# Optimization experiments

Measured on AMD Instinct MI355X. Metric: run time of the kernel, lower is better.

## Reference

```python
import jax, jax.numpy as jnp
import numpy as np

B, L, D, H = 4, 4096, 1024, 16
Dh = D // H
DECAY_INIT, DECAY_RANGE = 5.0, 1.0
LN_EPS = 1e-5


def setup_inputs() -> dict:
    key = jax.random.key(0)
    ks = jax.random.split(key, 5)
    s = 1.0 / np.sqrt(D)
    x = jax.random.normal(ks[0], (B, L, D), dtype=jnp.float32)
    Wq = jax.random.normal(ks[1], (D, D), dtype=jnp.float32) * s
    Wv = jax.random.normal(ks[2], (D, D), dtype=jnp.float32) * s
    Wo = jax.random.normal(ks[3], (D, D), dtype=jnp.float32) * s
    Wg = jax.random.normal(ks[4], (D, D), dtype=jnp.float32) * s
    # per-head decay logits, matching __init__: 5.0 + 1.0 * h / H
    beta = DECAY_INIT + DECAY_RANGE * (jnp.arange(H, dtype=jnp.float32) / H)
    ln_gamma = jnp.ones((D,), dtype=jnp.float32)
    ln_beta = jnp.zeros((D,), dtype=jnp.float32)
    return {"x": x, "Wq": Wq, "Wv": Wv, "Wo": Wo, "Wg": Wg,
            "beta": beta, "ln_gamma": ln_gamma, "ln_beta": ln_beta}


def _retention_scan(v, lam):
    # v: (B,L,H,Dh), lam: (H,); s_t = lam * s_{t-1} + v_t  (s_{-1} = 0)
    a = jnp.broadcast_to(lam[None, None, :, None], v.shape)

    def combine(c1, c2):
        a1, b1 = c1
        a2, b2 = c2
        return a1 * a2, a2 * b1 + b2

    _, s = jax.lax.associative_scan(combine, (a, v), axis=1)
    return s


def _layernorm(x, gamma, beta):
    mu = jnp.mean(x, axis=-1, keepdims=True)
    var = jnp.mean(jnp.square(x - mu), axis=-1, keepdims=True)
    return (x - mu) * jax.lax.rsqrt(var + LN_EPS) * gamma + beta


def reference(x, Wq, Wv, Wo, Wg, beta, ln_gamma, ln_beta):
    b, l, d = x.shape
    # decay lambda per head: (1 - 2^-beta) clamped to (tiny, 1 - 1e-9)
    tiny = jnp.finfo(jnp.float32).tiny
    lam = jnp.clip(1.0 - jnp.exp2(-beta), tiny, 1.0 - 1e-9)
    q = (x @ Wq.T).reshape(b, l, H, Dh)
    v = (x @ Wv.T).reshape(b, l, H, Dh)
    state = _retention_scan(v, lam)             # (B,L,H,Dh)
    ret = (q * state).reshape(b, l, d)          # per-timestep retention readout
    y = _layernorm(ret, ln_gamma, ln_beta)
    g = jax.nn.silu(x @ Wg.T)                   # swish gate
    out = (y * g) @ Wo.T
    return out
```

## Files before the change

### kernel.cpp

```cpp
#include <hip/hip_runtime.h>
#include <hip/hip_bf16.h>
#include <cfloat>

#define BB 4
#define LL 4096
#define DD 1024
#define HH 16
#define DHH 64
#define MM (BB * LL)
#define LN_EPS 1e-5f
#define LDQVG 3072
#define SCC 16
#define NCHUNK (LL / SCC)

typedef __hip_bfloat16 bf16;
typedef __attribute__((ext_vector_type(8))) short short8;
typedef __attribute__((ext_vector_type(4))) float f32x4;

struct bf16x4 { bf16 a, b, c, d; };
struct alignas(16) bf8 { bf16 e[8]; };

__device__ __forceinline__ float b2f(bf16 u) {
    union { unsigned int i; float f; } c;
    c.i = ((unsigned int)__bfloat16_as_ushort(u)) << 16;
    return c.f;
}

__device__ __forceinline__ float lam_of(const float* beta, int head) {
    float lam = 1.0f - exp2f(-beta[head]);
    return fminf(fmaxf(lam, 1.1754944e-38f), 1.0f - 1e-9f);
}

__global__ __launch_bounds__(256) void cvt_all(const float* __restrict__ x,
                                               const float* __restrict__ wq,
                                               const float* __restrict__ wv,
                                               const float* __restrict__ wg,
                                               const float* __restrict__ wo,
                                               bf16* __restrict__ xb,
                                               bf16* __restrict__ wb) {
    const int blk = blockIdx.x;
    const float* src;
    bf16* dst;
    size_t off;
    if (blk < 16384) {
        src = x; dst = xb; off = (size_t)blk * 1024;
    } else {
        int wblk  = blk - 16384;
        int which = wblk >> 10;
        src = (which == 0) ? wq : (which == 1) ? wv : (which == 2) ? wg : wo;
        dst = wb + (size_t)which * 1048576;
        off = (size_t)(wblk & 1023) * 1024;
    }
    size_t i = off + threadIdx.x * 4;
    float4 f = *(const float4*)(src + i);
    bf16x4 o;
    o.a = __float2bfloat16(f.x);
    o.b = __float2bfloat16(f.y);
    o.c = __float2bfloat16(f.z);
    o.d = __float2bfloat16(f.w);
    *(bf16x4*)(dst + i) = o;
}

__device__ __forceinline__ void async16(const bf16* g, bf16* l) {
    __builtin_amdgcn_global_load_lds(
        (const __attribute__((address_space(1))) void*)g,
        (__attribute__((address_space(3))) void*)l,
        16, 0, 0);
}

template <typename OutT, int KK>
__global__ __launch_bounds__(256, 2) void gemm_ring(const bf16* __restrict__ A,
                                                    const bf16* __restrict__ Bm,
                                                    OutT* __restrict__ C,
                                                    int ldc) {
    constexpr int BK    = 32;
    constexpr int NT    = KK / BK;
    constexpr int ASLOT = 256 * BK;
    constexpr int BSLOT = 128 * BK;

    __shared__ alignas(16) bf16 sA[3 * ASLOT];
    __shared__ alignas(16) bf16 sB[3 * BSLOT];

    const int t    = threadIdx.x;
    const int lane = t & 63;
    const int wave = t >> 6;
    const int wm   = wave >> 1;
    const int wn   = wave & 1;
    const int bm   = blockIdx.x;
    const int bn   = blockIdx.y;

    const int srow = t >> 2;
    const int cswz = ((t & 3) ^ ((srow >> 1) & 3)) * 8;
    const bf16* gA = A  + (size_t)(bm * 256 + srow) * KK + cswz;
    const bf16* gB = Bm + (size_t)(bn * 128 + srow) * KK + cswz;
    const size_t rstep = (size_t)64 * KK;
    bf16* const lA = sA + t * 8;
    bf16* const lB = sB + t * 8;

    const int f16  = lane & 15;
    const int swz8 = ((lane >> 4) ^ ((f16 >> 1) & 3)) * 8;
    const bf16* const rdA0 = sA + (wm * 128 + f16) * BK + swz8;
    const bf16* const rdB0 = sB + (wn * 64  + f16) * BK + swz8;

    f32x4 acc[8][4] = {};

    int slR = 0,         slR2 = 0;
    int slS = 2 * ASLOT, slS2 = 2 * BSLOT;

#pragma unroll
    for (int j = 0; j < 4; ++j) async16(gA + j * rstep, lA + j * 2048);
#pragma unroll
    for (int j = 0; j < 2; ++j) async16(gB + j * rstep, lB + j * 2048);
    gA += BK; gB += BK;
#pragma unroll
    for (int j = 0; j < 4; ++j) async16(gA + j * rstep, lA + ASLOT + j * 2048);
#pragma unroll
    for (int j = 0; j < 2; ++j) async16(gB + j * rstep, lB + BSLOT + j * 2048);
    gA += BK; gB += BK;
    asm volatile("s_waitcnt vmcnt(6)" ::: "memory");
    __builtin_amdgcn_s_barrier();

#define TILE(DOSTAGE, VMN)                                                     \
  {                                                                            \
    short8 a[8], b[4];                                                         \
    a[0] = *(const short8*)(rdA0 + slR);                                       \
    _Pragma("unroll") for (int ni = 0; ni < 4; ++ni)                           \
        b[ni] = *(const short8*)(rdB0 + ni * 512 + slR2);                      \
    _Pragma("unroll") for (int mi = 1; mi < 8; ++mi)                           \
        a[mi] = *(const short8*)(rdA0 + mi * 512 + slR);                       \
    if (DOSTAGE) {                                                             \
      _Pragma("unroll") for (int j = 0; j < 4; ++j)                            \
          async16(gA + j * rstep, lA + slS + j * 2048);                        \
      _Pragma("unroll") for (int j = 0; j < 2; ++j)                            \
          async16(gB + j * rstep, lB + slS2 + j * 2048);                       \
      gA += BK; gB += BK;                                                      \
    }                                                                          \
    __builtin_amdgcn_s_setprio(1);                                             \
    _Pragma("unroll") for (int mi = 0; mi < 8; ++mi)                           \
      _Pragma("unroll") for (int ni = 0; ni < 4; ++ni)                         \
        acc[mi][ni] = __builtin_amdgcn_mfma_f32_16x16x32_bf16(                 \
            a[mi], b[ni], acc[mi][ni], 0, 0, 0);                               \
    __builtin_amdgcn_s_setprio(0);                                             \
    if ((VMN) == 6)      asm volatile("s_waitcnt vmcnt(6)" ::: "memory");      \
    else if ((VMN) == 0) asm volatile("s_waitcnt vmcnt(0)" ::: "memory");      \
    if ((VMN) >= 0) __builtin_amdgcn_s_barrier();                              \
    slR  = (slR  == 2 * ASLOT) ? 0 : slR  + ASLOT;                             \
    slR2 = (slR2 == 2 * BSLOT) ? 0 : slR2 + BSLOT;                             \
    slS  = (slS  == 2 * ASLOT) ? 0 : slS  + ASLOT;                             \
    slS2 = (slS2 == 2 * BSLOT) ? 0 : slS2 + BSLOT;                             \
  }

#pragma unroll 1
    for (int T = 0; T < NT - 2; ++T) {
        TILE(true, 6);
    }
    TILE(false, 0);
    TILE(false, -1);

#undef TILE

    const int col0 = bn * 128 + wn * 64 + (lane & 15);
    const int row0 = bm * 256 + wm * 128 + ((lane >> 4) * 4);
#pragma unroll
    for (int mi = 0; mi < 8; ++mi) {
#pragma unroll
        for (int ni = 0; ni < 4; ++ni) {
#pragma unroll
            for (int r = 0; r < 4; ++r) {
                int row = row0 + mi * 16 + r;
                C[(size_t)row * ldc + col0 + ni * 16] = (OutT)acc[mi][ni][r];
            }
        }
    }
}

__global__ __launch_bounds__(64) void scan_chunksum(const bf16* __restrict__ qvg,
                                                    const float* __restrict__ beta,
                                                    float* __restrict__ S) {
    const int c    = blockIdx.x;
    const int half = blockIdx.y;
    const int b    = blockIdx.z;
    const int tid  = threadIdx.x;
    const int dh0  = half * 512 + tid * 8;
    const float lam = lam_of(beta, dh0 >> 6);

    const bf16* vp = qvg + 1024 + ((size_t)(b * LL + c * SCC)) * LDQVG + dh0;

    float s[8] = {};
#pragma unroll
    for (int t = 0; t < SCC; ++t) {
        bf8 vv = *(const bf8*)(vp + (size_t)t * LDQVG);
#pragma unroll
        for (int j = 0; j < 8; ++j)
            s[j] = fmaf(s[j], lam, b2f(vv.e[j]));
    }

    float* sp = S + ((size_t)(b * NCHUNK + c)) * DD + dh0;
    float4 lo = {s[0], s[1], s[2], s[3]};
    float4 hi = {s[4], s[5], s[6], s[7]};
    *(float4*)(sp)     = lo;
    *(float4*)(sp + 4) = hi;
}

__global__ __launch_bounds__(64) void scan_carry(const float* __restrict__ S,
                                                 float* __restrict__ T,
                                                 const float* __restrict__ beta) {
    const int gid = blockIdx.x * 64 + threadIdx.x;
    const int b = gid >> 10;
    const int f = gid & 1023;
    const float lam  = lam_of(beta, f >> 6);
    const float lamC = powf(lam, (float)SCC);

    const size_t base = (size_t)b * NCHUNK * DD + f;

    float v[8];
#pragma unroll
    for (int j = 0; j < 8; ++j) v[j] = S[base + (size_t)j * DD];

    float t = 0.0f;
    for (int c0 = 0; c0 < NCHUNK; c0 += 8) {
        float cur[8];
#pragma unroll
        for (int j = 0; j < 8; ++j) cur[j] = v[j];
        if (c0 + 8 < NCHUNK) {
#pragma unroll
            for (int j = 0; j < 8; ++j)
                v[j] = S[base + (size_t)(c0 + 8 + j) * DD];
        }
#pragma unroll
        for (int j = 0; j < 8; ++j) {
            T[base + (size_t)(c0 + j) * DD] = t;
            t = fmaf(t, lamC, cur[j]);
        }
    }
}

__global__ __launch_bounds__(128) void scan_apply_ln(const bf16* __restrict__ qvg,
                                                     const float* __restrict__ beta,
                                                     const float* __restrict__ T,
                                                     const float* __restrict__ gamma,
                                                     const float* __restrict__ betaln,
                                                     bf16* __restrict__ z) {
    __shared__ bf16 lds_ret[SCC][DD];

    const int c   = blockIdx.x;
    const int b   = blockIdx.y;
    const int tid = threadIdx.x;
    const int f0  = tid * 8;
    const float lam = lam_of(beta, f0 >> 6);

    const float* tp = T + ((size_t)(b * NCHUNK + c)) * DD + f0;
    float4 lo = *(const float4*)(tp);
    float4 hi = *(const float4*)(tp + 4);
    float s[8] = {lo.x, lo.y, lo.z, lo.w, hi.x, hi.y, hi.z, hi.w};

    const bf16* qp = qvg + ((size_t)(b * LL + c * SCC)) * LDQVG + f0;
#pragma unroll
    for (int t = 0; t < SCC; ++t) {
        const size_t off = (size_t)t * LDQVG;
        bf8 vv = *(const bf8*)(qp + 1024 + off);
        bf8 qq = *(const bf8*)(qp + off);
        bf8 o;
#pragma unroll
        for (int j = 0; j < 8; ++j) {
            s[j] = fmaf(s[j], lam, b2f(vv.e[j]));
            o.e[j] = __float2bfloat16(b2f(qq.e[j]) * s[j]);
        }
        *(bf8*)(&lds_ret[t][f0]) = o;
    }
    __syncthreads();

    const int lane = tid & 63;
    const int wv   = tid >> 6;

    float gmA[8], btA[8], gmB[8], btB[8];
#pragma unroll
    for (int j = 0; j < 8; j += 4) {
        *(float4*)(gmA + j) = *(const float4*)(gamma  + lane * 8 + j);
        *(float4*)(btA + j) = *(const float4*)(betaln + lane * 8 + j);
        *(float4*)(gmB + j) = *(const float4*)(gamma  + 512 + lane * 8 + j);
        *(float4*)(btB + j) = *(const float4*)(betaln + 512 + lane * 8 + j);
    }

    for (int t = wv; t < SCC; t += 2) {
        bf8 rA = *(const bf8*)(&lds_ret[t][lane * 8]);
        bf8 rB = *(const bf8*)(&lds_ret[t][512 + lane * 8]);

        float xa[8], xb2[8];
        float sum = 0.f, sq = 0.f;
#pragma unroll
        for (int j = 0; j < 8; ++j) {
            xa[j]  = b2f(rA.e[j]);
            xb2[j] = b2f(rB.e[j]);
            sum += xa[j] + xb2[j];
            sq  += xa[j] * xa[j] + xb2[j] * xb2[j];
        }
#pragma unroll
        for (int off = 32; off >= 1; off >>= 1) {
            sum += __shfl_xor(sum, off, 64);
            sq  += __shfl_xor(sq,  off, 64);
        }
        const float mu   = sum * (1.0f / DD);
        const float var  = sq * (1.0f / DD) - mu * mu;
        const float rstd = rsqrtf(var + LN_EPS);

        const size_t row = (size_t)(b * LL + c * SCC + t);
        const bf16* gp = qvg + row * LDQVG + 2048 + lane * 8;
        bf8 gA = *(const bf8*)(gp);
        bf8 gB = *(const bf8*)(gp + 512);

        bf8 oA, oB;
#pragma unroll
        for (int j = 0; j < 8; ++j) {
            float ya = (xa[j]  - mu) * rstd * gmA[j] + btA[j];
            float yb = (xb2[j] - mu) * rstd * gmB[j] + btB[j];
            float ga = b2f(gA.e[j]);
            float gb = b2f(gB.e[j]);
            oA.e[j] = __float2bfloat16(ya * (ga / (1.0f + expf(-ga))));
            oB.e[j] = __float2bfloat16(yb * (gb / (1.0f + expf(-gb))));
        }
        bf16* zp = z + row * DD + lane * 8;
        *(bf8*)(zp)       = oA;
        *(bf8*)(zp + 512) = oB;
    }
}

extern "C" void kernel_launch(void* const* d_in, const int* in_sizes, int n_in,
                              void* d_out, int out_size, void* d_ws, size_t ws_size,
                              hipStream_t stream) {
    const float* x     = (const float*)d_in[0];
    const float* Wq    = (const float*)d_in[1];
    const float* Wv    = (const float*)d_in[2];
    const float* Wo    = (const float*)d_in[3];
    const float* Wg    = (const float*)d_in[4];
    const float* beta  = (const float*)d_in[5];
    const float* ln_g  = (const float*)d_in[6];
    const float* ln_b  = (const float*)d_in[7];
    float* out = (float*)d_out;

    char* ws = (char*)d_ws;
    bf16*  xb   = (bf16*)ws;
    float* Sbuf = (float*)ws;
    bf16*  wqb  = (bf16*)(ws + (size_t)32 * 1024 * 1024);
    float* Tbuf = (float*)(ws + (size_t)32 * 1024 * 1024);
    bf16*  wob  = wqb + 3 * 1048576;
    bf16*  qvg  = (bf16*)(ws + (size_t)40 * 1024 * 1024);
    bf16*  zb   = xb;

    cvt_all<<<dim3(16384 + 4096), dim3(256), 0, stream>>>(x, Wq, Wv, Wg, Wo, xb, wqb);

    gemm_ring<bf16, DD><<<dim3(MM / 256, LDQVG / 128), dim3(256), 0, stream>>>(
        xb, wqb, qvg, LDQVG);

    scan_chunksum<<<dim3(NCHUNK, 2, BB), dim3(64), 0, stream>>>(qvg, beta, Sbuf);
    scan_carry<<<dim3(64), dim3(64), 0, stream>>>(Sbuf, Tbuf, beta);
    scan_apply_ln<<<dim3(NCHUNK, BB), dim3(128), 0, stream>>>(
        qvg, beta, Tbuf, ln_g, ln_b, zb);

    gemm_ring<float, DD><<<dim3(MM / 256, DD / 128), dim3(256), 0, stream>>>(
        zb, wob, out, DD);
}
```

Measured before the change: 333.3 us.

## Load GEMM B operand directly from global memory and prefetch gate rows

The GEMM no longer stages the B (weight) tile through LDS. Each wave now reads its B fragments straight from global memory into registers every K-step, and the LDS ring keeps only A, with the wait counts adjusted to match. Separately, the LayerNorm/gate kernel loads all eight gate rows for each wave up front, before the normalisation loop, so those global loads overlap the compute. The changes cut LDS traffic and footprint, which may allow higher occupancy, but B loads now sit on the critical path with no multi-buffering and are duplicated across waves (wm). More registers are also needed to hold the prefetched gate rows.

```diff
diff --git a/kernel.cpp b/kernel.cpp
--- a/kernel.cpp
+++ b/kernel.cpp
@@ -76,10 +76,8 @@
     constexpr int BK    = 32;
     constexpr int NT    = KK / BK;
     constexpr int ASLOT = 256 * BK;
-    constexpr int BSLOT = 128 * BK;
 
     __shared__ alignas(16) bf16 sA[3 * ASLOT];
-    __shared__ alignas(16) bf16 sB[3 * BSLOT];
 
     const int t    = threadIdx.x;
     const int lane = t & 63;
@@ -91,68 +89,62 @@
 
     const int srow = t >> 2;
     const int cswz = ((t & 3) ^ ((srow >> 1) & 3)) * 8;
-    const bf16* gA = A  + (size_t)(bm * 256 + srow) * KK + cswz;
-    const bf16* gB = Bm + (size_t)(bn * 128 + srow) * KK + cswz;
+    const bf16* gA = A + (size_t)(bm * 256 + srow) * KK + cswz;
     const size_t rstep = (size_t)64 * KK;
     bf16* const lA = sA + t * 8;
-    bf16* const lB = sB + t * 8;
 
     const int f16  = lane & 15;
     const int swz8 = ((lane >> 4) ^ ((f16 >> 1) & 3)) * 8;
     const bf16* const rdA0 = sA + (wm * 128 + f16) * BK + swz8;
-    const bf16* const rdB0 = sB + (wn * 64  + f16) * BK + swz8;
+
+    const bf16* gB = Bm + (size_t)(bn * 128 + wn * 64 + f16) * KK
+                   + (size_t)((lane >> 4) * 8);
+    const size_t nstep = (size_t)16 * KK;
 
     f32x4 acc[8][4] = {};
 
-    int slR = 0,         slR2 = 0;
-    int slS = 2 * ASLOT, slS2 = 2 * BSLOT;
+    int slR = 0;
+    int slS = 2 * ASLOT;
 
 #pragma unroll
     for (int j = 0; j < 4; ++j) async16(gA + j * rstep, lA + j * 2048);
-#pragma unroll
-    for (int j = 0; j < 2; ++j) async16(gB + j * rstep, lB + j * 2048);
-    gA += BK; gB += BK;
+    gA += BK;
 #pragma unroll
     for (int j = 0; j < 4; ++j) async16(gA + j * rstep, lA + ASLOT + j * 2048);
-#pragma unroll
-    for (int j = 0; j < 2; ++j) async16(gB + j * rstep, lB + BSLOT + j * 2048);
-    gA += BK; gB += BK;
-    asm volatile("s_waitcnt vmcnt(6)" ::: "memory");
+    gA += BK;
+    asm volatile("s_waitcnt vmcnt(4)" ::: "memory");
     __builtin_amdgcn_s_barrier();
 
 #define TILE(DOSTAGE, VMN)                                                     \
   {                                                                            \
-    short8 a[8], b[4];                                                         \
-    a[0] = *(const short8*)(rdA0 + slR);                                       \
+    short8 b[4];                                                               \
     _Pragma("unroll") for (int ni = 0; ni < 4; ++ni)                           \
-        b[ni] = *(const short8*)(rdB0 + ni * 512 + slR2);                      \
-    _Pragma("unroll") for (int mi = 1; mi < 8; ++mi)                           \
+        b[ni] = *(const short8*)(gB + ni * nstep);                             \
+    gB += BK;                                                                  \
+    short8 a[8];                                                               \
+    _Pragma("unroll") for (int mi = 0; mi < 8; ++mi)                           \
         a[mi] = *(const short8*)(rdA0 + mi * 512 + slR);                       \
     if (DOSTAGE) {                                                             \
       _Pragma("unroll") for (int j = 0; j < 4; ++j)                            \
           async16(gA + j * rstep, lA + slS + j * 2048);                        \
-      _Pragma("unroll") for (int j = 0; j < 2; ++j)                            \
-          async16(gB + j * rstep, lB + slS2 + j * 2048);                       \
-      gA += BK; gB += BK;                                                      \
+      gA += BK;                                                                \
     }                                                                          \
     __builtin_amdgcn_s_setprio(1);                                             \
-    _Pragma("unroll") for (int mi = 0; mi < 8; ++mi)                           \
-      _Pragma("unroll") for (int ni = 0; ni < 4; ++ni)                         \
+    _Pragma("unroll") for (int ni = 0; ni < 4; ++ni)                           \
+      _Pragma("unroll") for (int mi = 0; mi < 8; ++mi)                         \
         acc[mi][ni] = __builtin_amdgcn_mfma_f32_16x16x32_bf16(                 \
             a[mi], b[ni], acc[mi][ni], 0, 0, 0);                               \
     __builtin_amdgcn_s_setprio(0);                                             \
-    if ((VMN) == 6)      asm volatile("s_waitcnt vmcnt(6)" ::: "memory");      \
+    if ((VMN) == 4)      asm volatile("s_waitcnt vmcnt(4)" ::: "memory");      \
     else if ((VMN) == 0) asm volatile("s_waitcnt vmcnt(0)" ::: "memory");      \
     if ((VMN) >= 0) __builtin_amdgcn_s_barrier();                              \
-    slR  = (slR  == 2 * ASLOT) ? 0 : slR  + ASLOT;                             \
-    slR2 = (slR2 == 2 * BSLOT) ? 0 : slR2 + BSLOT;                             \
-    slS  = (slS  == 2 * ASLOT) ? 0 : slS  + ASLOT;                             \
-    slS2 = (slS2 == 2 * BSLOT) ? 0 : slS2 + BSLOT;                             \
+    slR = (slR == 2 * ASLOT) ? 0 : slR + ASLOT;                                \
+    slS = (slS == 2 * ASLOT) ? 0 : slS + ASLOT;                                \
   }
 
 #pragma unroll 1
     for (int T = 0; T < NT - 2; ++T) {
-        TILE(true, 6);
+        TILE(true, 4);
     }
     TILE(false, 0);
     TILE(false, -1);
@@ -273,6 +265,15 @@
     const int lane = tid & 63;
     const int wv   = tid >> 6;
 
+    bf8 gAp[8], gBp[8];
+#pragma unroll
+    for (int i = 0; i < 8; ++i) {
+        const size_t row = (size_t)(b * LL + c * SCC + wv + 2 * i);
+        const bf16* gp = qvg + row * LDQVG + 2048 + lane * 8;
+        gAp[i] = *(const bf8*)(gp);
+        gBp[i] = *(const bf8*)(gp + 512);
+    }
+
     float gmA[8], btA[8], gmB[8], btB[8];
 #pragma unroll
     for (int j = 0; j < 8; j += 4) {
@@ -282,7 +283,9 @@
         *(float4*)(btB + j) = *(const float4*)(betaln + 512 + lane * 8 + j);
     }
 
-    for (int t = wv; t < SCC; t += 2) {
+#pragma unroll
+    for (int i = 0; i < 8; ++i) {
+        const int t = wv + 2 * i;
         bf8 rA = *(const bf8*)(&lds_ret[t][lane * 8]);
         bf8 rB = *(const bf8*)(&lds_ret[t][512 + lane * 8]);
 
@@ -304,21 +307,17 @@
         const float var  = sq * (1.0f / DD) - mu * mu;
         const float rstd = rsqrtf(var + LN_EPS);
 
-        const size_t row = (size_t)(b * LL + c * SCC + t);
-        const bf16* gp = qvg + row * LDQVG + 2048 + lane * 8;
-        bf8 gA = *(const bf8*)(gp);
-        bf8 gB = *(const bf8*)(gp + 512);
-
         bf8 oA, oB;
 #pragma unroll
         for (int j = 0; j < 8; ++j) {
             float ya = (xa[j]  - mu) * rstd * gmA[j] + btA[j];
             float yb = (xb2[j] - mu) * rstd * gmB[j] + btB[j];
-            float ga = b2f(gA.e[j]);
-            float gb = b2f(gB.e[j]);
+            float ga = b2f(gAp[i].e[j]);
+            float gb = b2f(gBp[i].e[j]);
             oA.e[j] = __float2bfloat16(ya * (ga / (1.0f + expf(-ga))));
             oB.e[j] = __float2bfloat16(yb * (gb / (1.0f + expf(-gb))));
         }
+        const size_t row = (size_t)(b * LL + c * SCC + t);
         bf16* zp = z + row * DD + lane * 8;
         *(bf8*)(zp)       = oA;
         *(bf8*)(zp + 512) = oB;
```

Result: slower. 388.8 us (+16.6%).

## Fuse chunk-sum scan into QVG GEMM epilogue and prefetch loads in scan kernels

Applied to the files above, without the earlier changes.

Computes the per-chunk decayed V sums directly from the GEMM accumulators in the QVG projection epilogue, using lambda-power weights and cross-lane shuffles. This removes the separate scan_chunksum kernel and its re-read of V from global memory. The chunk sums are staged in the output buffer, which the final GEMM later overwrites. It also widens the carry scan's prefetch depth from 8 to 16 chunks and software-pipelines the q/v/gate loads in scan_apply_ln, at the cost of more registers and a heavier GEMM epilogue.

```diff
diff --git a/kernel.cpp b/kernel.cpp
--- a/kernel.cpp
+++ b/kernel.cpp
@@ -72,7 +72,9 @@
 __global__ __launch_bounds__(256, 2) void gemm_ring(const bf16* __restrict__ A,
                                                     const bf16* __restrict__ Bm,
                                                     OutT* __restrict__ C,
-                                                    int ldc) {
+                                                    int ldc,
+                                                    float* __restrict__ Sout,
+                                                    const float* __restrict__ beta) {
     constexpr int BK    = 32;
     constexpr int NT    = KK / BK;
     constexpr int ASLOT = 256 * BK;
@@ -172,34 +174,35 @@
             }
         }
     }
-}
-
-__global__ __launch_bounds__(64) void scan_chunksum(const bf16* __restrict__ qvg,
-                                                    const float* __restrict__ beta,
-                                                    float* __restrict__ S) {
-    const int c    = blockIdx.x;
-    const int half = blockIdx.y;
-    const int b    = blockIdx.z;
-    const int tid  = threadIdx.x;
-    const int dh0  = half * 512 + tid * 8;
-    const float lam = lam_of(beta, dh0 >> 6);
-
-    const bf16* vp = qvg + 1024 + ((size_t)(b * LL + c * SCC)) * LDQVG + dh0;
-
-    float s[8] = {};
-#pragma unroll
-    for (int t = 0; t < SCC; ++t) {
-        bf8 vv = *(const bf8*)(vp + (size_t)t * LDQVG);
-#pragma unroll
-        for (int j = 0; j < 8; ++j)
-            s[j] = fmaf(s[j], lam, b2f(vv.e[j]));
-    }
-
-    float* sp = S + ((size_t)(b * NCHUNK + c)) * DD + dh0;
-    float4 lo = {s[0], s[1], s[2], s[3]};
-    float4 hi = {s[4], s[5], s[6], s[7]};
-    *(float4*)(sp)     = lo;
-    *(float4*)(sp + 4) = hi;
+
+    if (Sout && bn >= 8 && bn < 16) {
+        const int p0 = (lane >> 4) * 4;
+        const int bglob = bm >> 4;
+        const int c0 = ((bm & 15) * 16 + wm * 8);
+#pragma unroll
+        for (int ni = 0; ni < 4; ++ni) {
+            const int f = col0 + ni * 16 - 1024;
+            const float lam = lam_of(beta, f >> 6);
+            const float l2g = __log2f(lam);
+            float w[4];
+#pragma unroll
+            for (int r = 0; r < 4; ++r)
+                w[r] = exp2f((float)(15 - p0 - r) * l2g);
+#pragma unroll
+            for (int mi = 0; mi < 8; ++mi) {
+                float part = 0.0f;
+#pragma unroll
+                for (int r = 0; r < 4; ++r)
+                    part = fmaf(w[r], acc[mi][ni][r], part);
+                part += __shfl_xor(part, 16, 64);
+                part += __shfl_xor(part, 32, 64);
+                if (p0 == 0) {
+                    const int cg = c0 + mi;
+                    Sout[((size_t)bglob * NCHUNK + cg) * DD + f] = part;
+                }
+            }
+        }
+    }
 }
 
 __global__ __launch_bounds__(64) void scan_carry(const float* __restrict__ S,
@@ -213,22 +216,22 @@
 
     const size_t base = (size_t)b * NCHUNK * DD + f;
 
-    float v[8];
-#pragma unroll
-    for (int j = 0; j < 8; ++j) v[j] = S[base + (size_t)j * DD];
+    float v[16];
+#pragma unroll
+    for (int j = 0; j < 16; ++j) v[j] = S[base + (size_t)j * DD];
 
     float t = 0.0f;
-    for (int c0 = 0; c0 < NCHUNK; c0 += 8) {
-        float cur[8];
-#pragma unroll
-        for (int j = 0; j < 8; ++j) cur[j] = v[j];
-        if (c0 + 8 < NCHUNK) {
-#pragma unroll
-            for (int j = 0; j < 8; ++j)
-                v[j] = S[base + (size_t)(c0 + 8 + j) * DD];
-        }
-#pragma unroll
-        for (int j = 0; j < 8; ++j) {
+    for (int c0 = 0; c0 < NCHUNK; c0 += 16) {
+        float cur[16];
+#pragma unroll
+        for (int j = 0; j < 16; ++j) cur[j] = v[j];
+        if (c0 + 16 < NCHUNK) {
+#pragma unroll
+            for (int j = 0; j < 16; ++j)
+                v[j] = S[base + (size_t)(c0 + 16 + j) * DD];
+        }
+#pragma unroll
+        for (int j = 0; j < 16; ++j) {
             T[base + (size_t)(c0 + j) * DD] = t;
             t = fmaf(t, lamC, cur[j]);
         }
@@ -255,11 +258,16 @@
     float s[8] = {lo.x, lo.y, lo.z, lo.w, hi.x, hi.y, hi.z, hi.w};
 
     const bf16* qp = qvg + ((size_t)(b * LL + c * SCC)) * LDQVG + f0;
+    bf8 vv = *(const bf8*)(qp + 1024);
+    bf8 qq = *(const bf8*)(qp);
 #pragma unroll
     for (int t = 0; t < SCC; ++t) {
-        const size_t off = (size_t)t * LDQVG;
-        bf8 vv = *(const bf8*)(qp + 1024 + off);
-        bf8 qq = *(const bf8*)(qp + off);
+        bf8 vn, qn;
+        if (t + 1 < SCC) {
+            const size_t offn = (size_t)(t + 1) * LDQVG;
+            vn = *(const bf8*)(qp + 1024 + offn);
+            qn = *(const bf8*)(qp + offn);
+        }
         bf8 o;
 #pragma unroll
         for (int j = 0; j < 8; ++j) {
@@ -267,11 +275,21 @@
             o.e[j] = __float2bfloat16(b2f(qq.e[j]) * s[j]);
         }
         *(bf8*)(&lds_ret[t][f0]) = o;
+        if (t + 1 < SCC) { vv = vn; qq = qn; }
     }
     __syncthreads();
 
     const int lane = tid & 63;
     const int wv   = tid >> 6;
+
+    bf8 gAp[8], gBp[8];
+#pragma unroll
+    for (int i = 0; i < 8; ++i) {
+        const size_t row = (size_t)(b * LL + c * SCC + wv + 2 * i);
+        const bf16* gp = qvg + row * LDQVG + 2048 + lane * 8;
+        gAp[i] = *(const bf8*)(gp);
+        gBp[i] = *(const bf8*)(gp + 512);
+    }
 
     float gmA[8], btA[8], gmB[8], btB[8];
 #pragma unroll
@@ -282,7 +300,9 @@
         *(float4*)(btB + j) = *(const float4*)(betaln + 512 + lane * 8 + j);
     }
 
-    for (int t = wv; t < SCC; t += 2) {
+#pragma unroll
+    for (int i = 0; i < 8; ++i) {
+        const int t = wv + 2 * i;
         bf8 rA = *(const bf8*)(&lds_ret[t][lane * 8]);
         bf8 rB = *(const bf8*)(&lds_ret[t][512 + lane * 8]);
 
@@ -304,21 +324,17 @@
         const float var  = sq * (1.0f / DD) - mu * mu;
         const float rstd = rsqrtf(var + LN_EPS);
 
-        const size_t row = (size_t)(b * LL + c * SCC + t);
-        const bf16* gp = qvg + row * LDQVG + 2048 + lane * 8;
-        bf8 gA = *(const bf8*)(gp);
-        bf8 gB = *(const bf8*)(gp + 512);
-
         bf8 oA, oB;
 #pragma unroll
         for (int j = 0; j < 8; ++j) {
             float ya = (xa[j]  - mu) * rstd * gmA[j] + btA[j];
             float yb = (xb2[j] - mu) * rstd * gmB[j] + btB[j];
-            float ga = b2f(gA.e[j]);
-            float gb = b2f(gB.e[j]);
+            float ga = b2f(gAp[i].e[j]);
+            float gb = b2f(gBp[i].e[j]);
             oA.e[j] = __float2bfloat16(ya * (ga / (1.0f + expf(-ga))));
             oB.e[j] = __float2bfloat16(yb * (gb / (1.0f + expf(-gb))));
         }
+        const size_t row = (size_t)(b * LL + c * SCC + t);
         bf16* zp = z + row * DD + lane * 8;
         *(bf8*)(zp)       = oA;
         *(bf8*)(zp + 512) = oB;
@@ -340,23 +356,22 @@
 
     char* ws = (char*)d_ws;
     bf16*  xb   = (bf16*)ws;
-    float* Sbuf = (float*)ws;
     bf16*  wqb  = (bf16*)(ws + (size_t)32 * 1024 * 1024);
     float* Tbuf = (float*)(ws + (size_t)32 * 1024 * 1024);
     bf16*  wob  = wqb + 3 * 1048576;
     bf16*  qvg  = (bf16*)(ws + (size_t)40 * 1024 * 1024);
     bf16*  zb   = xb;
+    float* Sbuf = out;
 
     cvt_all<<<dim3(16384 + 4096), dim3(256), 0, stream>>>(x, Wq, Wv, Wg, Wo, xb, wqb);
 
     gemm_ring<bf16, DD><<<dim3(MM / 256, LDQVG / 128), dim3(256), 0, stream>>>(
-        xb, wqb, qvg, LDQVG);
-
-    scan_chunksum<<<dim3(NCHUNK, 2, BB), dim3(64), 0, stream>>>(qvg, beta, Sbuf);
+        xb, wqb, qvg, LDQVG, Sbuf, beta);
+
     scan_carry<<<dim3(64), dim3(64), 0, stream>>>(Sbuf, Tbuf, beta);
     scan_apply_ln<<<dim3(NCHUNK, BB), dim3(128), 0, stream>>>(
         qvg, beta, Tbuf, ln_g, ln_b, zb);
 
     gemm_ring<float, DD><<<dim3(MM / 256, DD / 128), dim3(256), 0, stream>>>(
-        zb, wob, out, DD);
-}
+        zb, wob, out, DD, nullptr, nullptr);
+}
```

New measurement: 329.6 us. No clear change (-1.1%).
